# Kernel optimization log

Hardware: AMD Instinct MI355X
Metric: run time of the kernel (lower is better)

Reference implementation:

```python
import jax, jax.numpy as jnp
import numpy as np

N_FFT = 512
HOP = 128
WIN = 512
Q = 0.1
PCT_WIN = 31
FREQ_WIN = 5
TIME_WIN = 9
STRENGTH = 0.35
THRESH = 1.5
TEMP = 0.15
MIN_MASK = 0.08


def _hann_periodic(n):
    # matches torch.hann_window(n) (periodic)
    return (0.5 * (1.0 - jnp.cos(2.0 * jnp.pi * jnp.arange(n) / n))).astype(jnp.float32)


def _stft(x, window):
    # x: (B, L) -> complex (B, F, T); center=True, reflect pad
    pad = N_FFT // 2
    xp = jnp.pad(x, ((0, 0), (pad, pad)), mode='reflect')
    T = 1 + (xp.shape[-1] - N_FFT) // HOP
    idx = (jnp.arange(T) * HOP)[:, None] + jnp.arange(N_FFT)  # (T, n_fft)
    frames = xp[:, idx] * window  # (B, T, n_fft)
    return jnp.fft.rfft(frames, axis=-1).transpose(0, 2, 1)  # (B, F, T)


def _istft(spec, window, length):
    # spec: (B, F, T) complex -> (B, length)
    frames = jnp.fft.irfft(spec.transpose(0, 2, 1), n=N_FFT, axis=-1) * window  # (B,T,n_fft)
    B, T, _ = frames.shape
    total = N_FFT + HOP * (T - 1)
    idx = ((jnp.arange(T) * HOP)[:, None] + jnp.arange(N_FFT)).ravel()
    out = jnp.zeros((B, total), frames.dtype).at[:, idx].add(frames.reshape(B, -1))
    wsq = jnp.zeros((total,), frames.dtype).at[idx].add(
        jnp.broadcast_to(window ** 2, (T, N_FFT)).ravel())
    out = out / jnp.maximum(wsq, 1e-11)
    pad = N_FFT // 2
    return out[:, pad:pad + length]


def _rolling_quantile(mag):
    # mag: (B, F, T); replicate pad + sliding window of PCT_WIN along time
    p = PCT_WIN // 2
    padded = jnp.pad(mag, ((0, 0), (0, 0), (p, p)), mode='edge')
    T = mag.shape[-1]
    windows = jnp.stack([padded[..., i:i + T] for i in range(PCT_WIN)], axis=-1)  # (B,F,T,W)
    return jnp.quantile(windows, Q, axis=-1)


def _avg_pool(x, k, axis):
    # stride-1 avg pool with zero pad k//2, count_include_pad=True (torch default)
    if k <= 1:
        return x
    p = k // 2
    pads = [(0, 0)] * x.ndim
    pads[axis] = (p, p)
    xp = jnp.pad(x, pads)
    n = x.shape[axis]
    acc = 0.0
    for i in range(k):
        sl = [slice(None)] * x.ndim
        sl[axis] = slice(i, i + n)
        acc = acc + xp[tuple(sl)]
    return acc / k


def setup_inputs() -> dict:
    key = jax.random.key(0)
    k1, k2 = jax.random.split(key)
    B, L = 16, 160000
    noisy = jax.random.normal(k1, (B, L), dtype=jnp.float32)
    enhanced = jax.random.normal(k2, (B, L), dtype=jnp.float32)
    return {"noisy": noisy, "enhanced": enhanced}


def reference(noisy, enhanced):
    length = enhanced.shape[-1]
    window = _hann_periodic(WIN)
    e_spec = _stft(enhanced, window)
    n_spec = _stft(noisy, window)
    e_mag = jnp.maximum(jnp.abs(e_spec), 1e-6)
    n_mag = jnp.maximum(jnp.abs(n_spec), 1e-6)
    # mode == 'sg_input_floor': source is the noisy magnitude
    floor = _rolling_quantile(n_mag)
    floor = _avg_pool(floor, FREQ_WIN, axis=-2)
    floor = _avg_pool(floor, TIME_WIN, axis=-1)
    floor = jnp.maximum(floor, 1e-6)
    mask = jax.nn.sigmoid((e_mag - THRESH * floor) / (TEMP * floor + 1e-6))
    final_mask = MIN_MASK + (1.0 - MIN_MASK) * (1.0 - STRENGTH + STRENGTH * mask)
    phase = e_spec / jnp.maximum(jnp.abs(e_spec), 1e-12)  # unit-phase, = polar(1, angle)
    gated_spec = (e_mag * final_mask).astype(jnp.float32) * phase
    return _istft(gated_spec, window, length)
```

## Files before the change

### kernel.cpp

```cpp
#include <hip/hip_runtime.h>
#include <math.h>

#define BATCH 16
#define LEN   160000
#define NFFT  512
#define HOP   128
#define NT    1251
#define NF    257
#define PADC  256
#define TWO_PI 6.28318530717958647692f
#define P(i) ((i) + ((i) >> 5))
#define FBUF 528
#define GSTR 264

__device__ __forceinline__ int reflect_idx(int j) {
    j = j < 0 ? -j : j;
    j = j >= LEN ? 2*LEN - 2 - j : j;
    return j;
}

__device__ __forceinline__ float hann(int n) {
    return 0.5f - 0.5f * __cosf(TWO_PI * (float)n * (1.0f / 512.0f));
}

struct T4 { float m0, m1, m2, m3; };

__device__ __forceinline__ void ins(T4& a, float v) {
    const float x0 = fminf(a.m0, v);  const float c0 = fmaxf(a.m0, v);
    const float x1 = fminf(a.m1, c0); const float c1 = fmaxf(a.m1, c0);
    const float x2 = fminf(a.m2, c1); const float c2 = fmaxf(a.m2, c1);
    const float x3 = fminf(a.m3, c2);
    a.m0 = x0; a.m1 = x1; a.m2 = x2; a.m3 = x3;
}

__device__ __forceinline__ T4 merge4(const T4& a, const T4& b) {
    const float l0 = fminf(a.m0, b.m3);
    const float l1 = fminf(a.m1, b.m2);
    const float l2 = fminf(a.m2, b.m1);
    const float l3 = fminf(a.m3, b.m0);
    const float t0 = fminf(l0, l2), t2 = fmaxf(l0, l2);
    const float t1 = fminf(l1, l3), t3 = fmaxf(l1, l3);
    T4 r;
    r.m0 = fminf(t0, t1); r.m1 = fmaxf(t0, t1);
    r.m2 = fminf(t2, t3); r.m3 = fmaxf(t2, t3);
    return r;
}

__device__ __forceinline__ T4 sort4(float a, float b, float c, float d) {
    const float x0 = fminf(a, b), x1 = fmaxf(a, b);
    const float x2 = fminf(c, d), x3 = fmaxf(c, d);
    const float y0 = fminf(x0, x2), y2 = fmaxf(x0, x2);
    const float y1 = fminf(x1, x3), y3 = fmaxf(x1, x3);
    T4 r; r.m0 = y0; r.m1 = fminf(y1, y2); r.m2 = fmaxf(y1, y2); r.m3 = y3;
    return r;
}

__device__ __forceinline__ void dft8(float vr[8], float vi[8], float sign) {
    const float K = 0.70710678118654752f;
    float ar=vr[0]+vr[4], ai=vi[0]+vi[4];
    float br=vr[0]-vr[4], bi=vi[0]-vi[4];
    float cr=vr[2]+vr[6], ci=vi[2]+vi[6];
    float dr=vr[2]-vr[6], di=vi[2]-vi[6];
    float er=vr[1]+vr[5], ei=vi[1]+vi[5];
    float fr=vr[1]-vr[5], fi=vi[1]-vi[5];
    float gr=vr[3]+vr[7], gi=vi[3]+vi[7];
    float hr=vr[3]-vr[7], hi=vi[3]-vi[7];
    const float W4dr = -sign*di, W4di = sign*dr;
    const float W4hr = -sign*hi, W4hi = sign*hr;
    const float E0r=ar+cr, E0i=ai+ci, E2r=ar-cr, E2i=ai-ci;
    const float E1r=br+W4dr, E1i=bi+W4di, E3r=br-W4dr, E3i=bi-W4di;
    const float O0r=er+gr, O0i=ei+gi, O2r=er-gr, O2i=ei-gi;
    const float O1r=fr+W4hr, O1i=fi+W4hi, O3r=fr-W4hr, O3i=fi-W4hi;
    const float T1r = K*(O1r - sign*O1i), T1i = K*(O1i + sign*O1r);
    const float T2r = -sign*O2i,          T2i = sign*O2r;
    const float T3r = K*(-O3r - sign*O3i), T3i = K*(-O3i + sign*O3r);
    vr[0]=E0r+O0r; vi[0]=E0i+O0i;  vr[4]=E0r-O0r; vi[4]=E0i-O0i;
    vr[1]=E1r+T1r; vi[1]=E1i+T1i;  vr[5]=E1r-T1r; vi[5]=E1i-T1i;
    vr[2]=E2r+T2r; vi[2]=E2i+T2i;  vr[6]=E2r-T2r; vi[6]=E2i-T2i;
    vr[3]=E3r+T3r; vi[3]=E3i+T3i;  vr[7]=E3r-T3r; vi[7]=E3i-T3i;
}

template<int NS>
__device__ __forceinline__ void fft_pass(float* R, float* I, int j, float sign) {
    float vr[8], vi[8];
    #pragma unroll
    for (int r = 0; r < 8; ++r) { vr[r] = R[P(j + 64*r)]; vi[r] = I[P(j + 64*r)]; }
    const float th = sign * (TWO_PI / (8.0f * (float)NS)) * (float)(j & (NS - 1));
    float w1r, w1i; __sincosf(th, &w1i, &w1r);
    float wr = w1r, wi = w1i;
    #pragma unroll
    for (int r = 1; r < 8; ++r) {
        const float tr = vr[r]*wr - vi[r]*wi;
        vi[r] = vr[r]*wi + vi[r]*wr; vr[r] = tr;
        const float nwr = wr*w1r - wi*w1i;
        wi = wr*w1i + wi*w1r; wr = nwr;
    }
    dft8(vr, vi, sign);
    const int base = ((j / NS) * (8 * NS)) + (j & (NS - 1));
    #pragma unroll
    for (int r = 0; r < 8; ++r) { R[P(base + r*NS)] = vr[r]; I[P(base + r*NS)] = vi[r]; }
}

__device__ __forceinline__ void fft_pass_last(const float* R, const float* I, int j,
                                              float sign, float vr[8], float vi[8]) {
    #pragma unroll
    for (int r = 0; r < 8; ++r) { vr[r] = R[P(j + 64*r)]; vi[r] = I[P(j + 64*r)]; }
    const float th = sign * (TWO_PI / 512.0f) * (float)j;
    float w1r, w1i; __sincosf(th, &w1i, &w1r);
    float wr = w1r, wi = w1i;
    #pragma unroll
    for (int r = 1; r < 8; ++r) {
        const float tr = vr[r]*wr - vi[r]*wi;
        vi[r] = vr[r]*wi + vi[r]*wr; vr[r] = tr;
        const float nwr = wr*w1r - wi*w1i;
        wi = wr*w1i + wi*w1r; wr = nwr;
    }
    dft8(vr, vi, sign);
}

__global__ __launch_bounds__(256, 4) void stft_kernel(const float* __restrict__ enh,
                                                      const float* __restrict__ noi,
                                                      float2* __restrict__ e_spec,
                                                      float*  __restrict__ n_mag) {
    __shared__ float Ar[4*FBUF], Ai[4*FBUF];
    const int tid = threadIdx.x;
    const int w = tid >> 6, j = tid & 63;
    const int tr_ = blockIdx.x * 4 + w;
    const bool live = tr_ < NT;
    const int t = live ? tr_ : NT - 1;
    const int b = blockIdx.y;
    float* ar = Ar + w*FBUF; float* ai = Ai + w*FBUF;

    {
        const int sbase = t * HOP - PADC;
        float vr[8], vi[8];
        if (sbase >= 0 && sbase + NFFT <= LEN) {
            const float* __restrict__ pe = enh + b * LEN + sbase;
            const float* __restrict__ pn = noi + b * LEN + sbase;
            #pragma unroll
            for (int r = 0; r < 8; ++r) {
                const int n = j + 64*r;
                const float wd = hann(n);
                vr[r] = pe[n] * wd;
                vi[r] = pn[n] * wd;
            }
        } else {
            const float* __restrict__ pe = enh + b * LEN;
            const float* __restrict__ pn = noi + b * LEN;
            #pragma unroll
            for (int r = 0; r < 8; ++r) {
                const int n = j + 64*r;
                const int idx = reflect_idx(sbase + n);
                const float wd = hann(n);
                vr[r] = pe[idx] * wd;
                vi[r] = pn[idx] * wd;
            }
        }
        dft8(vr, vi, -1.0f);
        #pragma unroll
        for (int r = 0; r < 8; ++r) { ar[P(8*j + r)] = vr[r]; ai[P(8*j + r)] = vi[r]; }
    }
    fft_pass<8>(ar, ai, j, -1.0f);
    float zr[8], zi[8];
    fft_pass_last(ar, ai, j, -1.0f, zr, zi);

    const int src = (64 - j) & 63;
    float pr[4], pi_[4];
    #pragma unroll
    for (int q = 4; q < 8; ++q) {
        pr[q-4]  = __shfl(zr[q], src);
        pi_[q-4] = __shfl(zi[q], src);
    }
    if (live) {
        const int obase = (b * NT + t) * NF;
        #pragma unroll
        for (int r = 0; r < 4; ++r) {
            const int kk = j + 64*r;
            const float yr = (j == 0) ? zr[(8 - r) & 7] : pr[3 - r];
            const float yi = (j == 0) ? zi[(8 - r) & 7] : pi_[3 - r];
            const float er = 0.5f*(zr[r] + yr), ei = 0.5f*(zi[r] - yi);
            const float nr = 0.5f*(zi[r] + yi), ni = 0.5f*(yr - zr[r]);
            e_spec[obase + kk] = make_float2(er, ei);
            n_mag[obase + kk] = fmaxf(sqrtf(nr*nr + ni*ni), 1e-6f);
        }
        if (j == 0) {
            e_spec[obase + 256] = make_float2(zr[4], 0.0f);
            n_mag[obase + 256] = fmaxf(fabsf(zi[4]), 1e-6f);
        }
    }
}

__global__ __launch_bounds__(256) void floor_kernel(const float* __restrict__ n_mag,
                                                    float* __restrict__ floor_) {
    __shared__ float q[24][GSTR];
    __shared__ float fq[24];
    const int tid = threadIdx.x;
    const int t0 = blockIdx.x * 16, b = blockIdx.y;
    const float* __restrict__ pb = n_mag + b * NT * NF;

    {
        float wv[54];
        #pragma unroll
        for (int r = 0; r < 54; ++r) {
            int tr = t0 - 19 + r;
            tr = tr < 0 ? 0 : (tr > NT - 1 ? NT - 1 : tr);
            wv[r] = pb[tr * NF + tid];
        }
        T4 ch[6];
        #pragma unroll
        for (int c = 0; c < 6; ++c)
            ch[c] = merge4(sort4(wv[8*c],   wv[8*c+1], wv[8*c+2], wv[8*c+3]),
                           sort4(wv[8*c+4], wv[8*c+5], wv[8*c+6], wv[8*c+7]));
        #pragma unroll
        for (int k = 0; k < 24; ++k) {
            const int c0 = (k + 7) >> 3;
            T4 m = merge4(merge4(ch[c0], ch[c0+1]), ch[c0+2]);
            #pragma unroll
            for (int jj = k; jj < 8*c0; ++jj) ins(m, wv[jj]);
            #pragma unroll
            for (int jj = 8*c0 + 24; jj < k + 31; ++jj) ins(m, wv[jj]);
            q[k][tid] = m.m3;
        }
    }
    if (tid < 24) {
        const int k = tid;
        T4 m; m.m0 = m.m1 = m.m2 = m.m3 = 3.4e38f;
        for (int dt = -15; dt <= 15; ++dt) {
            int tt = t0 - 4 + k + dt;
            tt = tt < 0 ? 0 : (tt > NT - 1 ? NT - 1 : tt);
            ins(m, pb[tt * NF + 256]);
        }
        q[k][256] = m.m3;
    }
    __syncthreads();

    float fp[24];
    {
        const int f = tid;
        #pragma unroll
        for (int k = 0; k < 24; ++k) {
            float acc = 0.0f;
            #pragma unroll
            for (int df = -2; df <= 2; ++df) {
                const int ff = f + df;
                if (ff >= 0 && ff < NF) acc += q[k][ff];
            }
            fp[k] = acc * (1.0f / 5.0f);
        }
    }
    if (tid < 24) {
        const int k = tid;
        fq[k] = (q[k][254] + q[k][255] + q[k][256]) * (1.0f / 5.0f);
    }
    __syncthreads();

    {
        const int f = tid;
        #pragma unroll
        for (int k = 0; k < 24; ++k) {
            const int tq = t0 - 4 + k;
            fp[k] = (tq >= 0 && tq < NT) ? fp[k] : 0.0f;
        }
        float acc = 0.0f;
        #pragma unroll
        for (int k = 0; k < 9; ++k) acc += fp[k];
        #pragma unroll
        for (int to = 0; to < 16; ++to) {
            const int t = t0 + to;
            if (t < NT)
                floor_[(b * NT + t) * NF + f] = fmaxf(acc * (1.0f / 9.0f), 1e-6f);
            if (to < 15) acc += fp[to + 9] - fp[to];
        }
    }
    if (tid < 16) {
        const int to = tid;
        const int t = t0 + to;
        if (t < NT) {
            float acc = 0.0f;
            #pragma unroll
            for (int k = 0; k < 9; ++k) {
                const int tq = t0 - 4 + to + k;
                acc += (tq >= 0 && tq < NT) ? fq[to + k] : 0.0f;
            }
            floor_[(b * NT + t) * NF + 256] = fmaxf(acc * (1.0f / 9.0f), 1e-6f);
        }
    }
}

__global__ __launch_bounds__(256, 4) void istft_kernel(const float2* __restrict__ g,
                                                       const float* __restrict__ floor_,
                                                       float* __restrict__ frames) {
    __shared__ float gr[8*GSTR], gi[8*GSTR];
    const int tid = threadIdx.x;
    const int w = tid >> 6, j = tid & 63;
    const int t0 = blockIdx.x * 8, b = blockIdx.y;
    const int ta = t0 + 2*w, tb = ta + 1;

    float* g0r = gr + (2*w) * GSTR;      float* g0i = gi + (2*w) * GSTR;
    float* g1r = gr + (2*w + 1) * GSTR;  float* g1i = gi + (2*w + 1) * GSTR;

    for (int e = j; e < 2 * NF; e += 64) {
        const int h = (e >= NF) ? 1 : 0;
        const int kk = e - h * NF;
        const int t = ta + h;
        float grv = 0.0f, giv = 0.0f;
        if (t < NT) {
            const int idx = (b * NT + t) * NF + kk;
            const float fl = floor_[idx];
            const float2 e2 = g[idx];
            const float a = sqrtf(e2.x * e2.x + e2.y * e2.y);
            const float emag = fmaxf(a, 1e-6f);
            const float xarg = (emag - 1.5f * fl) / (0.15f * fl + 1e-6f);
            const float mask = 1.0f / (1.0f + __expf(-xarg));
            const float fm = 0.08f + 0.92f * (0.65f + 0.35f * mask);
            const float scale = emag * fm / fmaxf(a, 1e-12f);
            grv = e2.x * scale; giv = e2.y * scale;
        }
        gr[(2*w + h) * GSTR + kk] = grv;
        gi[(2*w + h) * GSTR + kk] = giv;
    }

    float* ar = g0r;
    float* ai = g0i;

    {
        float vr[8], vi[8];
        #pragma unroll
        for (int r = 0; r < 8; ++r) {
            const int n = j + 64*r;
            float cr, ci;
            if (n <= 256) {
                cr = g0r[n] - g1i[n];
                ci = g0i[n] + g1r[n];
            } else {
                const int m = 512 - n;
                cr = g0r[m] + g1i[m];
                ci = g1r[m] - g0i[m];
            }
            vr[r] = cr; vi[r] = ci;
        }
        dft8(vr, vi, 1.0f);
        #pragma unroll
        for (int r = 0; r < 8; ++r) { ar[P(8*j + r)] = vr[r]; ai[P(8*j + r)] = vi[r]; }
    }
    fft_pass<8>(ar, ai, j, 1.0f);
    float xr[8], xi[8];
    fft_pass_last(ar, ai, j, 1.0f, xr, xi);

    #pragma unroll
    for (int r = 0; r < 8; ++r) {
        const int n = j + 64*r;
        const float wd = hann(n) * (1.0f / 512.0f);
        if (ta < NT) frames[(b * NT + ta) * NFFT + n] = xr[r] * wd;
        if (tb < NT) frames[(b * NT + tb) * NFFT + n] = xi[r] * wd;
    }
}

__global__ __launch_bounds__(256) void ola_kernel(const float* __restrict__ frames,
                                                  float* __restrict__ out) {
    const int gid = blockIdx.x * 256 + threadIdx.x;
    if (gid >= BATCH * (LEN / 4)) return;
    const int b = gid / (LEN / 4);
    const int jj = (gid - b * (LEN / 4)) * 4;
    const int i = jj + PADC;
    const int q = i >> 7;
    const int n0 = i & 127;
    if (q >= 3 && q <= NT - 1) {
        const float* __restrict__ fp = frames + (b * NT + q) * NFFT + n0;
        const float4 a0 = *(const float4*)(fp);
        const float4 a1 = *(const float4*)(fp - 384);
        const float4 a2 = *(const float4*)(fp - 768);
        const float4 a3 = *(const float4*)(fp - 1152);
        float4 o;
        o.x = (a0.x + a1.x + a2.x + a3.x) * (2.0f / 3.0f);
        o.y = (a0.y + a1.y + a2.y + a3.y) * (2.0f / 3.0f);
        o.z = (a0.z + a1.z + a2.z + a3.z) * (2.0f / 3.0f);
        o.w = (a0.w + a1.w + a2.w + a3.w) * (2.0f / 3.0f);
        *(float4*)(out + b * LEN + jj) = o;
    } else {
        #pragma unroll
        for (int e = 0; e < 4; ++e) {
            const int ie = i + e;
            int t_lo = (ie >= 384) ? ((ie - 384) >> 7) : 0;
            int t_hi = ie >> 7; if (t_hi > NT - 1) t_hi = NT - 1;
            float acc = 0.0f, wacc = 0.0f;
            for (int t = t_lo; t <= t_hi; ++t) {
                const int n = ie - (t << 7);
                const float wd = hann(n);
                acc  += frames[(b * NT + t) * NFFT + n];
                wacc += wd * wd;
            }
            out[b * LEN + jj + e] = acc / fmaxf(wacc, 1e-11f);
        }
    }
}

extern "C" void kernel_launch(void* const* d_in, const int* in_sizes, int n_in,
                              void* d_out, int out_size, void* d_ws, size_t ws_size,
                              hipStream_t stream) {
    const float* noisy    = (const float*)d_in[0];
    const float* enhanced = (const float*)d_in[1];
    float* out = (float*)d_out;

    float* ws = (float*)d_ws;
    float2* e_spec = (float2*)ws;
    float* floor_ = ws + 10288224;
    float* n_mag  = ws + 15432336;
    float* frames = ws + 15432336;

    stft_kernel <<<dim3((NT + 3) / 4, BATCH), dim3(256), 0, stream>>>(enhanced, noisy, e_spec, n_mag);
    floor_kernel<<<dim3((NT + 15) / 16, BATCH), dim3(256), 0, stream>>>(n_mag, floor_);
    istft_kernel<<<dim3((NT + 7) / 8, BATCH), dim3(256), 0, stream>>>(e_spec, floor_, frames);
    ola_kernel  <<<dim3((BATCH * (LEN / 4) + 255) / 256), dim3(256), 0, stream>>>(frames, out);
}
```

Before: 145.3 us.

## Fuse iSTFT and overlap-add into one kernel with shared-memory frames and atomics

The iSTFT kernel now keeps its windowed output frames in shared memory and performs the overlap-add itself. Output samples fully covered by the block's 8 frames are stored directly, and boundary samples shared with neighbouring blocks are accumulated with atomicAdd. This removes the global frames buffer round trip and the separate OLA launch. In exchange it adds a memset of the output, atomics at block edges, and a scalar non-vectorized output loop.

```diff
diff --git a/kernel.cpp b/kernel.cpp
--- a/kernel.cpp
+++ b/kernel.cpp
@@ -287,9 +287,9 @@
     }
 }
 
-__global__ __launch_bounds__(256, 4) void istft_kernel(const float2* __restrict__ g,
-                                                       const float* __restrict__ floor_,
-                                                       float* __restrict__ frames) {
+__global__ __launch_bounds__(256, 4) void istft_ola_kernel(const float2* __restrict__ g,
+                                                           const float* __restrict__ floor_,
+                                                           float* __restrict__ out) {
     __shared__ float gr[8*GSTR], gi[8*GSTR];
     const int tid = threadIdx.x;
     const int w = tid >> 6, j = tid & 63;
@@ -351,47 +351,40 @@
     for (int r = 0; r < 8; ++r) {
         const int n = j + 64*r;
         const float wd = hann(n) * (1.0f / 512.0f);
-        if (ta < NT) frames[(b * NT + ta) * NFFT + n] = xr[r] * wd;
-        if (tb < NT) frames[(b * NT + tb) * NFFT + n] = xi[r] * wd;
-    }
-}
-
-__global__ __launch_bounds__(256) void ola_kernel(const float* __restrict__ frames,
-                                                  float* __restrict__ out) {
-    const int gid = blockIdx.x * 256 + threadIdx.x;
-    if (gid >= BATCH * (LEN / 4)) return;
-    const int b = gid / (LEN / 4);
-    const int jj = (gid - b * (LEN / 4)) * 4;
-    const int i = jj + PADC;
-    const int q = i >> 7;
-    const int n0 = i & 127;
-    if (q >= 3 && q <= NT - 1) {
-        const float* __restrict__ fp = frames + (b * NT + q) * NFFT + n0;
-        const float4 a0 = *(const float4*)(fp);
-        const float4 a1 = *(const float4*)(fp - 384);
-        const float4 a2 = *(const float4*)(fp - 768);
-        const float4 a3 = *(const float4*)(fp - 1152);
-        float4 o;
-        o.x = (a0.x + a1.x + a2.x + a3.x) * (2.0f / 3.0f);
-        o.y = (a0.y + a1.y + a2.y + a3.y) * (2.0f / 3.0f);
-        o.z = (a0.z + a1.z + a2.z + a3.z) * (2.0f / 3.0f);
-        o.w = (a0.w + a1.w + a2.w + a3.w) * (2.0f / 3.0f);
-        *(float4*)(out + b * LEN + jj) = o;
-    } else {
-        #pragma unroll
-        for (int e = 0; e < 4; ++e) {
-            const int ie = i + e;
-            int t_lo = (ie >= 384) ? ((ie - 384) >> 7) : 0;
-            int t_hi = ie >> 7; if (t_hi > NT - 1) t_hi = NT - 1;
-            float acc = 0.0f, wacc = 0.0f;
-            for (int t = t_lo; t <= t_hi; ++t) {
-                const int n = ie - (t << 7);
-                const float wd = hann(n);
-                acc  += frames[(b * NT + t) * NFFT + n];
+        ar[P(n)] = xr[r] * wd;
+        ai[P(n)] = xi[r] * wd;
+    }
+    __syncthreads();
+
+    const int i0 = t0 << 7;
+    for (int s = tid; s < 1408; s += 256) {
+        const int i = i0 + s;
+        const int jj = i - PADC;
+        if (jj < 0 || jj >= LEN) continue;
+        const int tl = (i >= 384) ? ((i - 384) >> 7) : 0;
+        int th = i >> 7; if (th > NT - 1) th = NT - 1;
+        const int ca = tl > t0 ? tl : t0;
+        const int cb = th < t0 + 7 ? th : t0 + 7;
+        if (cb < ca) continue;
+        float acc = 0.0f;
+        for (int t = ca; t <= cb; ++t) {
+            const int ft = t - t0;
+            const int n = i - (t << 7);
+            acc += ((ft & 1) ? gi : gr)[(ft >> 1) * FBUF + P(n)];
+        }
+        float winv;
+        if (th - tl == 3) winv = (2.0f / 3.0f);
+        else {
+            float wacc = 0.0f;
+            for (int t = tl; t <= th; ++t) {
+                const float wd = hann(i - (t << 7));
                 wacc += wd * wd;
             }
-            out[b * LEN + jj + e] = acc / fmaxf(wacc, 1e-11f);
-        }
+            winv = 1.0f / fmaxf(wacc, 1e-11f);
+        }
+        const float v = acc * winv;
+        if (tl >= t0 && th <= t0 + 7) out[b * LEN + jj] = v;
+        else atomicAdd(out + b * LEN + jj, v);
     }
 }
 
@@ -406,10 +399,9 @@
     float2* e_spec = (float2*)ws;
     float* floor_ = ws + 10288224;
     float* n_mag  = ws + 15432336;
-    float* frames = ws + 15432336;
 
     stft_kernel <<<dim3((NT + 3) / 4, BATCH), dim3(256), 0, stream>>>(enhanced, noisy, e_spec, n_mag);
     floor_kernel<<<dim3((NT + 15) / 16, BATCH), dim3(256), 0, stream>>>(n_mag, floor_);
-    istft_kernel<<<dim3((NT + 7) / 8, BATCH), dim3(256), 0, stream>>>(e_spec, floor_, frames);
-    ola_kernel  <<<dim3((BATCH * (LEN / 4) + 255) / 256), dim3(256), 0, stream>>>(frames, out);
-}
+    hipMemsetAsync(out, 0, (size_t)BATCH * LEN * sizeof(float), stream);
+    istft_ola_kernel<<<dim3((NT + 7) / 8, BATCH), dim3(256), 0, stream>>>(e_spec, floor_, out);
+}
```

Result: no change. 142.7 us (-1.8%).
